# Performance work log

Hardware: AMD Instinct MI355X
Metric: run time of the kernel (lower is better)

## Reference

```python
import jax, jax.numpy as jnp
import numpy as np

B, S, DM, TD, H, HD = 2, 2048, 1024, 1024, 16, 64


def setup_inputs() -> dict:
    key = jax.random.key(0)
    k1, k2, k3, k4 = jax.random.split(key, 4)
    query = jax.random.normal(k1, (B, S, DM), dtype=jnp.float32)
    # fused QKV projection weight (nn.Linear weight layout: [out, in]) and output proj
    W_in = jax.random.normal(k2, (3 * TD, DM), dtype=jnp.float32) * 0.02
    W_out = jax.random.normal(k3, (DM, TD), dtype=jnp.float32) * 0.02
    # standard RoPE tables, broadcastable against [B, H, S, HD]
    inv_freq = 1.0 / (10000.0 ** (jnp.arange(0, HD, 2, dtype=jnp.float32) / HD))
    t = jnp.arange(S, dtype=jnp.float32)
    freqs = jnp.outer(t, inv_freq)                      # [S, HD/2]
    emb = jnp.concatenate([freqs, freqs], axis=-1)      # [S, HD]
    sin_q = jnp.sin(emb)[None, None]                    # [1,1,S,HD]
    cos_q = jnp.cos(emb)[None, None]
    # padding mask over keys: first length[b] positions valid (>= S/2 so no NaN rows)
    lengths = jax.random.randint(k4, (B,), S // 2, S + 1)
    attn_mask = jnp.arange(S)[None, :] < lengths[:, None]  # [B, S] bool
    return {"query": query, "W_in": W_in, "W_out": W_out,
            "sin_q": sin_q, "cos_q": cos_q, "attn_mask": attn_mask}


def _rotate_half(x):
    x1, x2 = jnp.split(x, 2, axis=-1)
    return jnp.concatenate([-x2, x1], axis=-1)


def reference(query, W_in, W_out, sin_q, cos_q, attn_mask):
    # fused QKV projection (proj_in, bias=False)
    qkv = query @ W_in.T                                # [B, S, 3*TD]
    q, k, v = jnp.split(qkv, 3, axis=-1)
    to_heads = lambda x: x.reshape(B, S, H, HD).transpose(0, 2, 1, 3)  # [B,H,S,HD]
    q, k, v = to_heads(q), to_heads(k), to_heads(v)
    # RoPE (prefix = 0 since sin covers full sequence)
    q = q * cos_q + _rotate_half(q) * sin_q
    k = k * cos_q + _rotate_half(k) * sin_q
    # SDPA with padding-mask bias + causal mask
    scale = 1.0 / jnp.sqrt(jnp.float32(HD))
    scores = jnp.einsum('bhqd,bhkd->bhqk', q, k) * scale  # [B,H,S,S]
    causal = jnp.arange(S)[:, None] >= jnp.arange(S)[None, :]  # [S, S]
    mask = attn_mask[:, None, None, :] & causal[None, None]    # [B,1,S,S]
    scores = jnp.where(mask, scores, -jnp.inf)
    attn = jax.nn.softmax(scores, axis=-1)
    out = jnp.einsum('bhqk,bhkd->bhqd', attn, v)        # [B,H,S,HD]
    out = out.transpose(0, 2, 1, 3).reshape(B, S, TD)
    return out @ W_out.T                                 # [B, S, DM]
```

## Files before the change

kernel.cpp:

```cpp
#include <hip/hip_runtime.h>
#include <hip/hip_bf16.h>

#define B_ 2
#define S_ 2048
#define DM_ 1024
#define TD_ 1024
#define H_ 16
#define HD_ 64

using bf16 = __hip_bfloat16;
typedef __attribute__((ext_vector_type(8))) short s8v;
typedef __attribute__((ext_vector_type(4))) float f4v;

__device__ __forceinline__ f4v mfma_bf16(s8v a, s8v b, f4v c) {
    return __builtin_amdgcn_mfma_f32_16x16x32_bf16(a, b, c, 0, 0, 0);
}

__device__ __forceinline__ unsigned short f2bf(float f) {
    union { float f; unsigned int u; } v; v.f = f;
    unsigned int r = v.u + 0x7FFFu + ((v.u >> 16) & 1u);
    return (unsigned short)(r >> 16);
}

__device__ __forceinline__ int2 pack4bf(float a, float b, float c, float d) {
    int2 r;
    r.x = (int)((unsigned)f2bf(a) | ((unsigned)f2bf(b) << 16));
    r.y = (int)((unsigned)f2bf(c) | ((unsigned)f2bf(d) << 16));
    return r;
}

__device__ __forceinline__ bool detect_f32(const unsigned int* __restrict__ cosw) {
    return (cosw[0] & 0xFFFFu) == 0u;
}

__device__ __forceinline__ float ld_f(const void* p, int idx, bool f32) {
    return f32 ? ((const float*)p)[idx]
               : __bfloat162float(((const bf16*)p)[idx]);
}

__device__ __forceinline__ void gload_lds16(const bf16* g, void* l) {
    __builtin_amdgcn_global_load_lds(
        (const __attribute__((address_space(1))) unsigned int*)(const void*)g,
        (__attribute__((address_space(3))) unsigned int*)l,
        16, 0, 0);
}

#define NQ_  (B_ * S_ * DM_)
#define NWI_ (3 * TD_ * DM_)
#define NWO_ (DM_ * TD_)
__global__ __launch_bounds__(256)
void cvt_all(const void* __restrict__ q, const void* __restrict__ wi,
             const void* __restrict__ wo, bf16* __restrict__ dst,
             const unsigned int* __restrict__ cosw) {
    const bool f32 = detect_f32(cosw);
    int i = (blockIdx.x * 256 + threadIdx.x) * 8;
    const void* src; int off;
    if (i < NQ_)              { src = q;  off = i; }
    else if (i < NQ_ + NWI_)  { src = wi; off = i - NQ_; }
    else                      { src = wo; off = i - NQ_ - NWI_; }
    if (f32) {
        const float* p = (const float*)src + off;
        float4 x = *reinterpret_cast<const float4*>(p);
        float4 y = *reinterpret_cast<const float4*>(p + 4);
        union { unsigned short u[8]; int4 v; } t;
        t.u[0] = f2bf(x.x); t.u[1] = f2bf(x.y); t.u[2] = f2bf(x.z); t.u[3] = f2bf(x.w);
        t.u[4] = f2bf(y.x); t.u[5] = f2bf(y.y); t.u[6] = f2bf(y.z); t.u[7] = f2bf(y.w);
        *reinterpret_cast<int4*>(dst + i) = t.v;
    } else {
        *reinterpret_cast<int4*>(dst + i) =
            *reinterpret_cast<const int4*>((const bf16*)src + off);
    }
}

__global__ __launch_bounds__(256)
void compute_lengths(const void* __restrict__ mask, int* __restrict__ lengths) {
    int b = blockIdx.x;
    unsigned int w0 = ((const unsigned int*)mask)[0];
    int enc;
    if (w0 == 1u) enc = 0;
    else if (w0 == 0x01010101u) enc = 1;
    else if (w0 == 0x3F803F80u) enc = 2;
    else enc = 3;
    int cnt = 0;
    for (int s = threadIdx.x; s < S_; s += 256) {
        int i = b * S_ + s;
        bool v;
        if (enc == 0)      v = ((const int*)mask)[i] != 0;
        else if (enc == 1) v = ((const unsigned char*)mask)[i] != 0;
        else if (enc == 2) v = ((const unsigned short*)mask)[i] != 0;
        else               v = ((const float*)mask)[i] != 0.f;
        cnt += v ? 1 : 0;
    }
    __shared__ int red[256];
    red[threadIdx.x] = cnt;
    __syncthreads();
    for (int off = 128; off > 0; off >>= 1) {
        if (threadIdx.x < off) red[threadIdx.x] += red[threadIdx.x + off];
        __syncthreads();
    }
    if (threadIdx.x == 0) lengths[b] = red[0];
}

__global__ __launch_bounds__(256)
void gemm_nt(const bf16* __restrict__ A, const bf16* __restrict__ Bm,
             void* __restrict__ C, int M, int N, int K,
             int c_dyn, const unsigned int* __restrict__ cosw) {
    __shared__ bf16 lds_a[128 * 64];
    __shared__ bf16 lds_b[128 * 64];

    const bool cf32 = c_dyn && detect_f32(cosw);

    const int t = threadIdx.x;
    const int wave = t >> 6, lane = t & 63;
    const int quad = lane >> 4, l16 = lane & 15;
    const int wm = wave >> 1, wn = wave & 1;
    const int m0 = blockIdx.y * 128, n0 = blockIdx.x * 128;
    const int wuni = __builtin_amdgcn_readfirstlane(wave);

    f4v acc[4][4];
    #pragma unroll
    for (int i = 0; i < 4; i++)
        #pragma unroll
        for (int j = 0; j < 4; j++)
            acc[i][j] = f4v{0.f, 0.f, 0.f, 0.f};

    for (int k0 = 0; k0 < K; k0 += 64) {
        __syncthreads();
        #pragma unroll
        for (int i = 0; i < 4; i++) {
            int ci = i * 256 + t;
            int row = ci >> 3;
            int csrc = (ci & 7) ^ (row & 7);
            gload_lds16(A + (size_t)(m0 + row) * K + k0 + csrc * 8,
                        (char*)lds_a + i * 4096 + wuni * 1024);
            gload_lds16(Bm + (size_t)(n0 + row) * K + k0 + csrc * 8,
                        (char*)lds_b + i * 4096 + wuni * 1024);
        }
        __syncthreads();

        #pragma unroll
        for (int kk = 0; kk < 2; kk++) {
            s8v afr[4], bfr[4];
            #pragma unroll
            for (int mb = 0; mb < 4; mb++) {
                int r = wm * 64 + mb * 16 + l16;
                int ch = (kk * 4 + quad) ^ (l16 & 7);
                afr[mb] = *reinterpret_cast<const s8v*>(&lds_a[r * 64 + ch * 8]);
            }
            #pragma unroll
            for (int nb = 0; nb < 4; nb++) {
                int r = wn * 64 + nb * 16 + l16;
                int ch = (kk * 4 + quad) ^ (l16 & 7);
                bfr[nb] = *reinterpret_cast<const s8v*>(&lds_b[r * 64 + ch * 8]);
            }
            #pragma unroll
            for (int mb = 0; mb < 4; mb++)
                #pragma unroll
                for (int nb = 0; nb < 4; nb++)
                    acc[mb][nb] = mfma_bf16(bfr[nb], afr[mb], acc[mb][nb]);
        }
    }

    #pragma unroll
    for (int mb = 0; mb < 4; mb++) {
        int m = m0 + wm * 64 + mb * 16 + l16;
        #pragma unroll
        for (int nb = 0; nb < 4; nb++) {
            int n = n0 + wn * 64 + nb * 16 + quad * 4;
            f4v v = acc[mb][nb];
            if (cf32) {
                *reinterpret_cast<f4v*>(&((float*)C)[(size_t)m * N + n]) = v;
            } else {
                *reinterpret_cast<int2*>(&((bf16*)C)[(size_t)m * N + n]) =
                    pack4bf(v[0], v[1], v[2], v[3]);
            }
        }
    }
}

__global__ __launch_bounds__(256)
void rope_split(const bf16* __restrict__ qkv,
                const void* __restrict__ sin_t, const void* __restrict__ cos_t,
                bf16* __restrict__ Qh, bf16* __restrict__ Kt) {
    const bool f32 = detect_f32((const unsigned int*)cos_t);
    int idx = blockIdx.x * 256 + threadIdx.x;
    int d = idx & 63;
    int h = (idx >> 6) & 15;
    int s = (idx >> 10) & 2047;
    int b = idx >> 21;
    size_t row = (size_t)(b * S_ + s) * 3072;
    int col  = h * 64 + d;
    int colp = h * 64 + ((d + 32) & 63);
    float sgn = (d < 32) ? -1.f : 1.f;
    float cs = ld_f(cos_t, s * 64 + d, f32);
    float sn = ld_f(sin_t, s * 64 + d, f32);
    float q  = __bfloat162float(qkv[row + col]);
    float qp = __bfloat162float(qkv[row + colp]);
    float k  = __bfloat162float(qkv[row + 1024 + col]);
    float kp = __bfloat162float(qkv[row + 1024 + colp]);
    Qh[((size_t)((b * H_ + h) * S_ + s)) * 64 + d] =
        __float2bfloat16((q * cs + sgn * qp * sn) * 0.180336880f);
    size_t ktile = ((size_t)(b * H_ + h) * 32 + (s >> 6)) * 4096;
    int dp = ((((d >> 3) ^ (s & 7)) << 3) | (d & 7));
    Kt[ktile + (s & 63) * 64 + dp] = __float2bfloat16(k * cs + sgn * kp * sn);
}

__global__ __launch_bounds__(256)
void v_transpose(const bf16* __restrict__ qkv, bf16* __restrict__ Vt) {
    __shared__ bf16 tile[64 * 72];
    const int t = threadIdx.x;
    const int sb = blockIdx.x, h = blockIdx.y, b = blockIdx.z;
    #pragma unroll
    for (int i = 0; i < 2; i++) {
        int id = i * 256 + t;
        int row = id >> 3, c = id & 7;
        *reinterpret_cast<int4*>(&tile[row * 72 + c * 8]) =
            *reinterpret_cast<const int4*>(
                qkv + (size_t)(b * S_ + sb * 64 + row) * 3072 + 2048 + h * 64 + c * 8);
    }
    __syncthreads();
    const size_t tb = ((size_t)(b * H_ + h) * 32 + sb) * 4096;
    #pragma unroll
    for (int i = 0; i < 2; i++) {
        int id = i * 256 + t;
        int d = id >> 3, kc = id & 7;
        union { short s[8]; int4 v; } u;
        #pragma unroll
        for (int e = 0; e < 8; e++)
            u.s[e] = reinterpret_cast<const short*>(tile)[(kc * 8 + e) * 72 + d];
        *reinterpret_cast<int4*>(Vt + tb + d * 64 + ((kc ^ (d & 7)) * 8)) = u.v;
    }
}

__global__ __launch_bounds__(256)
void attn_fused(const bf16* __restrict__ Qh, const bf16* __restrict__ Kt,
                const bf16* __restrict__ Vt, const int* __restrict__ lengths,
                bf16* __restrict__ out) {
    __shared__ bf16 k_buf[2 * 4096];
    __shared__ bf16 v_buf[2 * 4096];
    __shared__ bf16 lds_p[4 * 16 * 72];

    const int t = threadIdx.x, wave = t >> 6, lane = t & 63;
    const int quad = lane >> 4, l16 = lane & 15;
    const int bid = blockIdx.x;
    const int slot = bid >> 3;
    const int bh = (bid & 7) * 4 + (slot >> 5);
    const int qb = slot & 31;
    const int b = bh >> 4, h = bh & 15;

    const size_t hb = (size_t)bh * S_ * 64;
    const bf16* Ktp = Kt + (size_t)bh * 32 * 4096;
    const bf16* Vtp = Vt + (size_t)bh * 32 * 4096;
    const int wuni = __builtin_amdgcn_readfirstlane(wave);
    int len_raw = lengths[b];
    const int len_b = len_raw < 1 ? 1 : (len_raw > S_ ? S_ : len_raw);

    const int qbase = qb * 64;
    const int qrow_g = qbase + wave * 16 + l16;
    const int kmax = (qrow_g < len_b - 1) ? qrow_g : (len_b - 1);

    s8v qf[2];
    {
        const bf16* qptr = Qh + hb + (size_t)qrow_g * 64 + quad * 8;
        qf[0] = *reinterpret_cast<const s8v*>(qptr);
        qf[1] = *reinterpret_cast<const s8v*>(qptr + 32);
    }

    f4v o_acc[4];
    #pragma unroll
    for (int a = 0; a < 4; a++) o_acc[a] = f4v{0.f, 0.f, 0.f, 0.f};
    float l_sum = 0.f;

    const int nkt_len = (len_b + 63) >> 6;
    const int nkt = (qb + 1) < nkt_len ? (qb + 1) : nkt_len;

    #pragma unroll
    for (int i = 0; i < 2; i++) {
        int ci = i * 256 + t;
        gload_lds16(Ktp + ci * 8, (char*)k_buf + i * 4096 + wuni * 1024);
        gload_lds16(Vtp + ci * 8, (char*)v_buf + i * 4096 + wuni * 1024);
    }

    for (int kt = 0; kt < nkt; kt++) {
        const int kbase = kt * 64;
        const int cur = kt & 1;
        __syncthreads();

        if (kt + 1 < nkt) {
            const bf16* kst = Ktp + (size_t)(kt + 1) * 4096;
            const bf16* vst = Vtp + (size_t)(kt + 1) * 4096;
            int bo = (cur ^ 1) * 8192;
            #pragma unroll
            for (int i = 0; i < 2; i++) {
                int ci = i * 256 + t;
                gload_lds16(kst + ci * 8, (char*)k_buf + bo + i * 4096 + wuni * 1024);
                gload_lds16(vst + ci * 8, (char*)v_buf + bo + i * 4096 + wuni * 1024);
            }
        }

        const bf16* kb = k_buf + cur * 4096;
        const bf16* vb = v_buf + cur * 4096;

        f4v s_acc[4];
        #pragma unroll
        for (int a = 0; a < 4; a++) s_acc[a] = f4v{0.f, 0.f, 0.f, 0.f};
        #pragma unroll
        for (int kk = 0; kk < 2; kk++) {
            #pragma unroll
            for (int a = 0; a < 4; a++) {
                int ch = (kk * 4 + quad) ^ (l16 & 7);
                s8v kf = *reinterpret_cast<const s8v*>(
                    &kb[(a * 16 + l16) * 64 + ch * 8]);
                s_acc[a] = mfma_bf16(kf, qf[kk], s_acc[a]);
            }
        }

        const bool tail = (kt == qb) || (kbase + 64 > len_b);
        #pragma unroll
        for (int a = 0; a < 4; a++) {
            float p0[4];
            #pragma unroll
            for (int r = 0; r < 4; r++) {
                float e = __builtin_amdgcn_exp2f(s_acc[a][r]);
                if (tail) {
                    int key = kbase + a * 16 + quad * 4 + r;
                    e = (key <= kmax) ? e : 0.f;
                }
                p0[r] = e;
                l_sum += e;
            }
            *reinterpret_cast<int2*>(
                &lds_p[(wave * 16 + l16) * 72 + a * 16 + quad * 4]) =
                pack4bf(p0[0], p0[1], p0[2], p0[3]);
        }

        asm volatile("s_waitcnt lgkmcnt(0)" ::: "memory");

        #pragma unroll
        for (int kk = 0; kk < 2; kk++) {
            s8v pf = *reinterpret_cast<const s8v*>(
                &lds_p[(wave * 16 + l16) * 72 + kk * 32 + quad * 8]);
            #pragma unroll
            for (int a = 0; a < 4; a++) {
                int ch = (kk * 4 + quad) ^ (l16 & 7);
                s8v vf = *reinterpret_cast<const s8v*>(
                    &vb[(a * 16 + l16) * 64 + ch * 8]);
                o_acc[a] = mfma_bf16(vf, pf, o_acc[a]);
            }
        }
    }

    l_sum += __shfl_xor(l_sum, 16);
    l_sum += __shfl_xor(l_sum, 32);
    float inv_l = 1.f / l_sum;
    size_t orow = ((size_t)(b * S_ + qrow_g)) * TD_ + h * 64;
    #pragma unroll
    for (int a = 0; a < 4; a++) {
        *reinterpret_cast<int2*>(&out[orow + a * 16 + quad * 4]) =
            pack4bf(o_acc[a][0] * inv_l, o_acc[a][1] * inv_l,
                    o_acc[a][2] * inv_l, o_acc[a][3] * inv_l);
    }
}

extern "C" void kernel_launch(void* const* d_in, const int* in_sizes, int n_in,
                              void* d_out, int out_size, void* d_ws, size_t ws_size,
                              hipStream_t stream) {
    const void* query = d_in[0];
    const void* W_in  = d_in[1];
    const void* W_out = d_in[2];
    const void* sin_q = d_in[3];
    const void* cos_q = d_in[4];
    const void* mask  = d_in[5];
    const unsigned int* cosw = (const unsigned int*)cos_q;

    const size_t nQ  = NQ_;
    const size_t nWi = NWI_;
    const size_t nWo = NWO_;

    bf16* qkv  = (bf16*)d_ws;
    bf16* Qh   = qkv + (size_t)4096 * 3072;
    bf16* Kt   = Qh + nQ;
    bf16* qbf  = Kt + nQ;
    bf16* wibf = qbf + nQ;
    bf16* wobf = wibf + nWi;
    int* lengths = (int*)(wobf + nWo);
    bf16* Vt   = qbf;
    bf16* attn = qkv;

    compute_lengths<<<B_, 256, 0, stream>>>(mask, lengths);
    cvt_all<<<(int)((nQ + nWi + nWo) / (256 * 8)), 256, 0, stream>>>(
        query, W_in, W_out, qbf, cosw);

    dim3 g1(3072 / 128, 4096 / 128);
    gemm_nt<<<g1, 256, 0, stream>>>(qbf, wibf, qkv, 4096, 3072, 1024, 0, cosw);

    rope_split<<<(B_ * S_ * H_ * HD_) / 256, 256, 0, stream>>>(qkv, sin_q, cos_q, Qh, Kt);
    dim3 gv(S_ / 64, H_, B_);
    v_transpose<<<gv, 256, 0, stream>>>(qkv, Vt);

    attn_fused<<<1024, 256, 0, stream>>>(Qh, Kt, Vt, lengths, attn);

    dim3 g2(1024 / 128, 4096 / 128);
    gemm_nt<<<g2, 256, 0, stream>>>(attn, wobf, d_out, 4096, 1024, 1024, 1, cosw);
}
```

Before: 216.0 us.

## Software-pipeline attention loop: overlap QK MFMA of tile k with softmax/PV of tile k-1

The attention inner loop is restructured so the QK^T MFMAs for the current key tile are issued before the exp/P·V work for the previous tile. This lets the matrix and vector work interleave. V tiles are now loaded one iteration later than K tiles, and the barrier moves to the end of each iteration. Separately, the manual float-to-bf16 rounding is replaced with the hardware packed conversion instruction v_cvt_pk_bf16_f32. The pipelining keeps an extra set of score registers live, which raises register pressure, and the V buffer reuse timing is now more delicate.

```diff
diff --git a/kernel.cpp b/kernel.cpp
--- a/kernel.cpp
+++ b/kernel.cpp
@@ -16,16 +16,15 @@
     return __builtin_amdgcn_mfma_f32_16x16x32_bf16(a, b, c, 0, 0, 0);
 }
 
-__device__ __forceinline__ unsigned short f2bf(float f) {
-    union { float f; unsigned int u; } v; v.f = f;
-    unsigned int r = v.u + 0x7FFFu + ((v.u >> 16) & 1u);
-    return (unsigned short)(r >> 16);
-}
-
+__device__ __forceinline__ unsigned cvt_pk_bf16(float a, float b) {
+    unsigned r;
+    asm("v_cvt_pk_bf16_f32 %0, %1, %2" : "=v"(r) : "v"(a), "v"(b));
+    return r;
+}
 __device__ __forceinline__ int2 pack4bf(float a, float b, float c, float d) {
     int2 r;
-    r.x = (int)((unsigned)f2bf(a) | ((unsigned)f2bf(b) << 16));
-    r.y = (int)((unsigned)f2bf(c) | ((unsigned)f2bf(d) << 16));
+    r.x = (int)cvt_pk_bf16(a, b);
+    r.y = (int)cvt_pk_bf16(c, d);
     return r;
 }
 
@@ -62,9 +61,11 @@
         const float* p = (const float*)src + off;
         float4 x = *reinterpret_cast<const float4*>(p);
         float4 y = *reinterpret_cast<const float4*>(p + 4);
-        union { unsigned short u[8]; int4 v; } t;
-        t.u[0] = f2bf(x.x); t.u[1] = f2bf(x.y); t.u[2] = f2bf(x.z); t.u[3] = f2bf(x.w);
-        t.u[4] = f2bf(y.x); t.u[5] = f2bf(y.y); t.u[6] = f2bf(y.z); t.u[7] = f2bf(y.w);
+        union { unsigned u[4]; int4 v; } t;
+        t.u[0] = cvt_pk_bf16(x.x, x.y);
+        t.u[1] = cvt_pk_bf16(x.z, x.w);
+        t.u[2] = cvt_pk_bf16(y.x, y.y);
+        t.u[3] = cvt_pk_bf16(y.z, y.w);
         *reinterpret_cast<int4*>(dst + i) = t.v;
     } else {
         *reinterpret_cast<int4*>(dst + i) =
@@ -274,33 +275,71 @@
     const int nkt_len = (len_b + 63) >> 6;
     const int nkt = (qb + 1) < nkt_len ? (qb + 1) : nkt_len;
 
+    f4v s_prev[4];
+    auto process_tile = [&](int pt, const bf16* vb) {
+        const int pbase = pt * 64;
+        const bool tail = (pt == qb) || (pbase + 64 > len_b);
+        #pragma unroll
+        for (int a = 0; a < 4; a++) {
+            float e0[4];
+            #pragma unroll
+            for (int r = 0; r < 4; r++) {
+                float e = __builtin_amdgcn_exp2f(s_prev[a][r]);
+                if (tail) {
+                    int key = pbase + a * 16 + quad * 4 + r;
+                    e = (key <= kmax) ? e : 0.f;
+                }
+                e0[r] = e;
+                l_sum += e;
+            }
+            *reinterpret_cast<int2*>(
+                &lds_p[(wave * 16 + l16) * 72 + a * 16 + quad * 4]) =
+                pack4bf(e0[0], e0[1], e0[2], e0[3]);
+        }
+        asm volatile("s_waitcnt lgkmcnt(0)" ::: "memory");
+        #pragma unroll
+        for (int kk = 0; kk < 2; kk++) {
+            s8v pf = *reinterpret_cast<const s8v*>(
+                &lds_p[(wave * 16 + l16) * 72 + kk * 32 + quad * 8]);
+            #pragma unroll
+            for (int a = 0; a < 4; a++) {
+                int ch = (kk * 4 + quad) ^ (l16 & 7);
+                s8v vf = *reinterpret_cast<const s8v*>(
+                    &vb[(a * 16 + l16) * 64 + ch * 8]);
+                o_acc[a] = mfma_bf16(vf, pf, o_acc[a]);
+            }
+        }
+    };
+
     #pragma unroll
     for (int i = 0; i < 2; i++) {
         int ci = i * 256 + t;
         gload_lds16(Ktp + ci * 8, (char*)k_buf + i * 4096 + wuni * 1024);
-        gload_lds16(Vtp + ci * 8, (char*)v_buf + i * 4096 + wuni * 1024);
-    }
+    }
+    __syncthreads();
 
     for (int kt = 0; kt < nkt; kt++) {
-        const int kbase = kt * 64;
         const int cur = kt & 1;
-        __syncthreads();
-
+        {
+            const bf16* vst = Vtp + (size_t)kt * 4096;
+            #pragma unroll
+            for (int i = 0; i < 2; i++) {
+                int ci = i * 256 + t;
+                gload_lds16(vst + ci * 8,
+                            (char*)v_buf + cur * 8192 + i * 4096 + wuni * 1024);
+            }
+        }
         if (kt + 1 < nkt) {
             const bf16* kst = Ktp + (size_t)(kt + 1) * 4096;
-            const bf16* vst = Vtp + (size_t)(kt + 1) * 4096;
-            int bo = (cur ^ 1) * 8192;
             #pragma unroll
             for (int i = 0; i < 2; i++) {
                 int ci = i * 256 + t;
-                gload_lds16(kst + ci * 8, (char*)k_buf + bo + i * 4096 + wuni * 1024);
-                gload_lds16(vst + ci * 8, (char*)v_buf + bo + i * 4096 + wuni * 1024);
+                gload_lds16(kst + ci * 8,
+                            (char*)k_buf + (cur ^ 1) * 8192 + i * 4096 + wuni * 1024);
             }
         }
 
         const bf16* kb = k_buf + cur * 4096;
-        const bf16* vb = v_buf + cur * 4096;
-
         f4v s_acc[4];
         #pragma unroll
         for (int a = 0; a < 4; a++) s_acc[a] = f4v{0.f, 0.f, 0.f, 0.f};
@@ -315,40 +354,14 @@
             }
         }
 
-        const bool tail = (kt == qb) || (kbase + 64 > len_b);
-        #pragma unroll
-        for (int a = 0; a < 4; a++) {
-            float p0[4];
-            #pragma unroll
-            for (int r = 0; r < 4; r++) {
-                float e = __builtin_amdgcn_exp2f(s_acc[a][r]);
-                if (tail) {
-                    int key = kbase + a * 16 + quad * 4 + r;
-                    e = (key <= kmax) ? e : 0.f;
-                }
-                p0[r] = e;
-                l_sum += e;
-            }
-            *reinterpret_cast<int2*>(
-                &lds_p[(wave * 16 + l16) * 72 + a * 16 + quad * 4]) =
-                pack4bf(p0[0], p0[1], p0[2], p0[3]);
-        }
-
-        asm volatile("s_waitcnt lgkmcnt(0)" ::: "memory");
-
-        #pragma unroll
-        for (int kk = 0; kk < 2; kk++) {
-            s8v pf = *reinterpret_cast<const s8v*>(
-                &lds_p[(wave * 16 + l16) * 72 + kk * 32 + quad * 8]);
-            #pragma unroll
-            for (int a = 0; a < 4; a++) {
-                int ch = (kk * 4 + quad) ^ (l16 & 7);
-                s8v vf = *reinterpret_cast<const s8v*>(
-                    &vb[(a * 16 + l16) * 64 + ch * 8]);
-                o_acc[a] = mfma_bf16(vf, pf, o_acc[a]);
-            }
-        }
-    }
+        if (kt > 0) process_tile(kt - 1, v_buf + ((kt - 1) & 1) * 4096);
+
+        #pragma unroll
+        for (int a = 0; a < 4; a++) s_prev[a] = s_acc[a];
+
+        __syncthreads();
+    }
+    process_tile(nkt - 1, v_buf + ((nkt - 1) & 1) * 4096);
 
     l_sum += __shfl_xor(l_sum, 16);
     l_sum += __shfl_xor(l_sum, 32);
```

After: 206.8 us. -4.3%, faster.
